# Kernel tuning notes

Measured on AMD Instinct MI355X. Metric: run time of the kernel, lower is better.

## Reference

```python
import jax, jax.numpy as jnp
import numpy as np

D = 1024
H = 16
HD = D // H


def setup_inputs() -> dict:
    key = jax.random.key(0)
    ks = jax.random.split(key, 9)
    s = 1.0 / np.sqrt(D)
    x = jax.random.normal(ks[0], (2, 2048, D), dtype=jnp.float32)
    Wq = jax.random.uniform(ks[1], (D, D), jnp.float32, -s, s)
    bq = jax.random.uniform(ks[2], (D,), jnp.float32, -s, s)
    Wk = jax.random.uniform(ks[3], (D, D), jnp.float32, -s, s)
    bk = jax.random.uniform(ks[4], (D,), jnp.float32, -s, s)
    Wv = jax.random.uniform(ks[5], (D, D), jnp.float32, -s, s)
    bv = jax.random.uniform(ks[6], (D,), jnp.float32, -s, s)
    Wo = jax.random.uniform(ks[7], (D, D), jnp.float32, -s, s)
    bo = jax.random.uniform(ks[8], (D,), jnp.float32, -s, s)
    return {"x": x, "Wq": Wq, "bq": bq, "Wk": Wk, "bk": bk,
            "Wv": Wv, "bv": bv, "Wo": Wo, "bo": bo}


def reference(x, Wq, bq, Wk, bk, Wv, bv, Wo, bo):
    B, S, _ = x.shape
    # project and split heads -> [B, H, S, HD]
    def split(t):
        return t.reshape(B, S, H, HD).transpose(0, 2, 1, 3)
    q = split(x @ Wq + bq)
    k = split(x @ Wk + bk)
    v = split(x @ Wv + bv)
    scores = jnp.einsum('bhqd,bhkd->bhqk', q, k) / np.sqrt(HD).astype(np.float32)
    attn = jax.nn.softmax(scores, axis=-1)
    ctx = jnp.einsum('bhqk,bhkd->bhqd', attn, v)  # [B,H,S,HD]
    ctx = ctx.transpose(0, 2, 1, 3).reshape(B, S, D)
    return ctx @ Wo + bo
```

## Files before the change

### kernel.cpp

```cpp
#include <hip/hip_runtime.h>
#include <hip/hip_bf16.h>
#include <math.h>

#define BB 2
#define SS 2048
#define DD 1024
#define HH 16
#define HD 64
#define MM (BB * SS)
#define NT (SS / 64)

typedef __bf16 bf16;
typedef __attribute__((ext_vector_type(8))) __bf16 bf16x8;
typedef __attribute__((ext_vector_type(4))) __bf16 bf16x4;
typedef __attribute__((ext_vector_type(4))) float f32x4;
typedef __attribute__((ext_vector_type(4))) unsigned u32x4;

#define QSCL 0.18033688011112042f

__device__ __forceinline__ void glds16(const bf16* g, bf16* l) {
    __builtin_amdgcn_global_load_lds(
        (const __attribute__((address_space(1))) void*)g,
        (__attribute__((address_space(3))) void*)l, 16, 0, 0);
}

__device__ __forceinline__ unsigned cvtpk_bf16(float a, float b) {
    unsigned r;
    asm("v_cvt_pk_bf16_f32 %0, %1, %2" : "=v"(r) : "v"(a), "v"(b));
    return r;
}

__global__ __launch_bounds__(256) void cvt_x(const float* __restrict__ x,
                                             bf16* __restrict__ xb) {
    int i = (blockIdx.x * 256 + threadIdx.x) * 4;
    float4 v = *(const float4*)(x + i);
    bf16x4 o;
    o[0] = (bf16)v.x; o[1] = (bf16)v.y; o[2] = (bf16)v.z; o[3] = (bf16)v.w;
    *(bf16x4*)(xb + i) = o;
}

__global__ __launch_bounds__(256) void cvt_w(
    const float* __restrict__ W0, const float* __restrict__ W1,
    const float* __restrict__ W2, const float* __restrict__ W3,
    bf16* __restrict__ Wt) {
    const float* W = (blockIdx.z == 0) ? W0 : (blockIdx.z == 1) ? W1
                   : (blockIdx.z == 2) ? W2 : W3;
    bf16* dst = Wt + (size_t)blockIdx.z * DD * DD;

    __shared__ float T[64][65];
    int k0 = blockIdx.y * 64, n0 = blockIdx.x * 64;
    int tr = threadIdx.x >> 4, tc = (threadIdx.x & 15) * 4;
#pragma unroll
    for (int u = 0; u < 4; u++) {
        int r = tr + u * 16;
        float4 v = *(const float4*)&W[(size_t)(k0 + r) * DD + n0 + tc];
        T[tc + 0][r] = v.x; T[tc + 1][r] = v.y;
        T[tc + 2][r] = v.z; T[tc + 3][r] = v.w;
    }
    __syncthreads();
#pragma unroll
    for (int u = 0; u < 4; u++) {
        int r = tr + u * 16;
        bf16x4 o;
        o[0] = (bf16)T[r][tc + 0]; o[1] = (bf16)T[r][tc + 1];
        o[2] = (bf16)T[r][tc + 2]; o[3] = (bf16)T[r][tc + 3];
        *(bf16x4*)&dst[(size_t)(n0 + r) * DD + k0 + tc] = o;
    }
}

__global__ __launch_bounds__(256) void vt_kernel(const bf16* __restrict__ V,
                                                 bf16* __restrict__ Vt) {
    const int bh = blockIdx.y;
    const int b = bh >> 4, h = bh & 15;
    const int s0 = blockIdx.x * 64;

    __shared__ bf16 T[64][72];
    const int r = threadIdx.x >> 2;
    const int C = threadIdx.x & 3;
    const int c0 = C * 16;

    const bf16* src = V + ((size_t)(b * SS + s0 + r)) * DD + h * HD + c0;
    *(bf16x8*)&T[r][c0]     = *(const bf16x8*)(src);
    *(bf16x8*)&T[r][c0 + 8] = *(const bf16x8*)(src + 8);
    __syncthreads();

    const int M0 = (C >> 1) * 32 + (C & 1) * 8;
    bf16x8 o0, o1;
#pragma unroll
    for (int i = 0; i < 4; i++) o0[i]     = T[M0 + i][r];
#pragma unroll
    for (int i = 0; i < 4; i++) o0[4 + i] = T[M0 + 16 + i][r];
#pragma unroll
    for (int i = 0; i < 4; i++) o1[i]     = T[M0 + 4 + i][r];
#pragma unroll
    for (int i = 0; i < 4; i++) o1[4 + i] = T[M0 + 20 + i][r];
    bf16* dst = Vt + ((size_t)bh * HD + r) * SS + s0 + c0;
    *(bf16x8*)dst       = o0;
    *(bf16x8*)(dst + 8) = o1;
}

__global__ __launch_bounds__(256) void mfma_gemm(
    const bf16* __restrict__ A, const bf16* __restrict__ Wt0,
    const float* __restrict__ b0, const float* __restrict__ b1,
    const float* __restrict__ b2,
    bf16* __restrict__ o0, bf16* __restrict__ o1, bf16* __restrict__ o2) {
    const int z = blockIdx.z;
    const bf16* Wt = Wt0 + (size_t)z * DD * DD;
    const float* bias = (z == 0) ? b0 : (z == 1) ? b1 : b2;
    bf16* dstb = (z == 0) ? o0 : (z == 1) ? o1 : o2;
    const float scl = (z == 0) ? QSCL : 1.0f;

    __shared__ __align__(16) bf16 As[128 * 64];
    __shared__ __align__(16) bf16 Bs[128 * 64];

    const int tid = threadIdx.x;
    const int lane = tid & 63;
    const int w = tid >> 6;
    const int l15 = lane & 15, quad = lane >> 4;
    const int m0 = blockIdx.y * 128;
    const int n0 = blockIdx.x * 128;
    const int mw = (w & 1) * 64;
    const int nw = (w >> 1) * 64;

    f32x4 acc[4][4];
#pragma unroll
    for (int i = 0; i < 4; i++)
#pragma unroll
        for (int j = 0; j < 4; j++) acc[i][j] = (f32x4){0.f, 0.f, 0.f, 0.f};

    for (int kt = 0; kt < DD; kt += 64) {
        __syncthreads();
#pragma unroll
        for (int u = 0; u < 4; u++) {
            int j = tid + u * 256;
            int row = j >> 3, cp = j & 7;
            int c = cp ^ (row & 7);
            glds16(A  + (size_t)(m0 + row) * DD + kt + c * 8, &As[j * 8]);
            glds16(Wt + (size_t)(n0 + row) * DD + kt + c * 8, &Bs[j * 8]);
        }
        __syncthreads();

#pragma unroll
        for (int kh = 0; kh < 2; kh++) {
            bf16x8 af[4], bf[4];
#pragma unroll
            for (int i = 0; i < 4; i++) {
                int ra = mw + i * 16 + l15;
                int ja = ra * 8 + ((kh * 4 + quad) ^ (ra & 7));
                af[i] = *(const bf16x8*)&As[ja * 8];
                int rb = nw + i * 16 + l15;
                int jb = rb * 8 + ((kh * 4 + quad) ^ (rb & 7));
                bf[i] = *(const bf16x8*)&Bs[jb * 8];
            }
#pragma unroll
            for (int i = 0; i < 4; i++)
#pragma unroll
                for (int j = 0; j < 4; j++)
                    acc[i][j] = __builtin_amdgcn_mfma_f32_16x16x32_bf16(
                        af[i], bf[j], acc[i][j], 0, 0, 0);
        }
    }

    float bcol[4];
#pragma unroll
    for (int j = 0; j < 4; j++) bcol[j] = bias[n0 + nw + j * 16 + l15];

#pragma unroll
    for (int i = 0; i < 4; i++)
#pragma unroll
        for (int j = 0; j < 4; j++)
#pragma unroll
            for (int r = 0; r < 4; r++) {
                int row = m0 + mw + i * 16 + quad * 4 + r;
                int col = n0 + nw + j * 16 + l15;
                dstb[(size_t)row * DD + col] =
                    (bf16)((acc[i][j][r] + bcol[j]) * scl);
            }
}

__global__ __launch_bounds__(256) void mfma_gemm_out(
    const bf16* __restrict__ A, const bf16* __restrict__ Wt,
    const float* __restrict__ bias, float* __restrict__ out) {
    __shared__ __align__(16) bf16 As[64 * 64];
    __shared__ __align__(16) bf16 Bs[128 * 64];

    const int tid = threadIdx.x;
    const int lane = tid & 63;
    const int w = tid >> 6;
    const int l15 = lane & 15, quad = lane >> 4;
    const int m0 = blockIdx.y * 64;
    const int n0 = blockIdx.x * 128;
    const int mw = (w & 1) * 32;
    const int nw = (w >> 1) * 64;

    f32x4 acc[2][4];
#pragma unroll
    for (int i = 0; i < 2; i++)
#pragma unroll
        for (int j = 0; j < 4; j++) acc[i][j] = (f32x4){0.f, 0.f, 0.f, 0.f};

    for (int kt = 0; kt < DD; kt += 64) {
        __syncthreads();
#pragma unroll
        for (int u = 0; u < 2; u++) {
            int j = tid + u * 256;
            int row = j >> 3, c = (j & 7) ^ (row & 7);
            glds16(A + (size_t)(m0 + row) * DD + kt + c * 8, &As[j * 8]);
        }
#pragma unroll
        for (int u = 0; u < 4; u++) {
            int j = tid + u * 256;
            int row = j >> 3, c = (j & 7) ^ (row & 7);
            glds16(Wt + (size_t)(n0 + row) * DD + kt + c * 8, &Bs[j * 8]);
        }
        __syncthreads();

#pragma unroll
        for (int kh = 0; kh < 2; kh++) {
            bf16x8 af[2], bf[4];
#pragma unroll
            for (int i = 0; i < 2; i++) {
                int ra = mw + i * 16 + l15;
                int ja = ra * 8 + ((kh * 4 + quad) ^ (ra & 7));
                af[i] = *(const bf16x8*)&As[ja * 8];
            }
#pragma unroll
            for (int j = 0; j < 4; j++) {
                int rb = nw + j * 16 + l15;
                int jb = rb * 8 + ((kh * 4 + quad) ^ (rb & 7));
                bf[j] = *(const bf16x8*)&Bs[jb * 8];
            }
#pragma unroll
            for (int i = 0; i < 2; i++)
#pragma unroll
                for (int j = 0; j < 4; j++)
                    acc[i][j] = __builtin_amdgcn_mfma_f32_16x16x32_bf16(
                        af[i], bf[j], acc[i][j], 0, 0, 0);
        }
    }

    float bcol[4];
#pragma unroll
    for (int j = 0; j < 4; j++) bcol[j] = bias[n0 + nw + j * 16 + l15];

#pragma unroll
    for (int i = 0; i < 2; i++)
#pragma unroll
        for (int j = 0; j < 4; j++)
#pragma unroll
            for (int r = 0; r < 4; r++) {
                int row = m0 + mw + i * 16 + quad * 4 + r;
                int col = n0 + nw + j * 16 + l15;
                out[(size_t)row * DD + col] = acc[i][j][r] + bcol[j];
            }
}

__global__ __launch_bounds__(256) void mfma_attn(
    const bf16* __restrict__ Qb, const bf16* __restrict__ Kb,
    const bf16* __restrict__ Vtg, bf16* __restrict__ ctxb) {
    __shared__ __align__(16) bf16 Ks[2][64 * 64];
    __shared__ __align__(16) bf16 Vs[2][64 * 64];

    const int tid = threadIdx.x;
    const int lane = tid & 63;
    const int w = tid >> 6;
    const int l15 = lane & 15, quad = lane >> 4;
    const int bh = blockIdx.y;
    const int b = bh >> 4, h = bh & 15;
    const int q0 = blockIdx.x * 64;
    const size_t mb = (size_t)b * SS;
    const int hc = h * HD;
    const bf16* Vt_bh = Vtg + (size_t)bh * HD * SS;

    bf16x8 qf[2];
#pragma unroll
    for (int kh = 0; kh < 2; kh++)
        qf[kh] = *(const bf16x8*)&Qb[(mb + q0 + w * 16 + l15) * DD +
                                     hc + kh * 32 + quad * 8];

    bf16x8 onev;
#pragma unroll
    for (int i = 0; i < 8; i++) onev[i] = (bf16)1.0f;

    int koff[4][2], voff[4][2];
#pragma unroll
    for (int kb = 0; kb < 4; kb++) {
        int rk = kb * 16 + l15;
#pragma unroll
        for (int kh = 0; kh < 2; kh++)
            koff[kb][kh] = (rk * 8 + ((kh * 4 + quad) ^ (rk & 7))) * 8;
    }
#pragma unroll
    for (int nb = 0; nb < 4; nb++) {
        int rv = nb * 16 + l15;
#pragma unroll
        for (int kh = 0; kh < 2; kh++)
            voff[nb][kh] = (rv * 8 + ((kh * 4 + quad) ^ (rv & 7))) * 8;
    }

    const bf16* gK[2]; const bf16* gV[2]; int lo_[2];
#pragma unroll
    for (int u = 0; u < 2; u++) {
        int j = tid + u * 256;
        int row = j >> 3, cp = j & 7;
        int c = cp ^ (row & 7);
        gK[u] = Kb + (mb + row) * DD + hc + c * 8;
        gV[u] = Vt_bh + (size_t)row * SS + c * 8;
        lo_[u] = j * 8;
    }

    f32x4 o[4], lsum;
    lsum = (f32x4){0.f, 0.f, 0.f, 0.f};
#pragma unroll
    for (int nb = 0; nb < 4; nb++) o[nb] = (f32x4){0.f, 0.f, 0.f, 0.f};

#pragma unroll
    for (int u = 0; u < 2; u++) {
        glds16(gK[u], &Ks[0][lo_[u]]);  gK[u] += 64 * DD;
        glds16(gV[u], &Vs[0][lo_[u]]);  gV[u] += 64;
    }
    __syncthreads();

    f32x4 scA[4];
#pragma unroll
    for (int kb = 0; kb < 4; kb++) scA[kb] = (f32x4){0.f, 0.f, 0.f, 0.f};
#pragma unroll
    for (int kb = 0; kb < 4; kb++)
#pragma unroll
        for (int kh = 0; kh < 2; kh++) {
            bf16x8 kf = *(const bf16x8*)&Ks[0][koff[kb][kh]];
            scA[kb] = __builtin_amdgcn_mfma_f32_16x16x32_bf16(
                kf, qf[kh], scA[kb], 0, 0, 0);
        }

    int buf = 0;
    for (int it = 0; it < NT; ++it) {
        const bool more = (it + 1 < NT);
        if (more) {
#pragma unroll
            for (int u = 0; u < 2; u++) {
                glds16(gK[u], &Ks[buf ^ 1][lo_[u]]);  gK[u] += 64 * DD;
                glds16(gV[u], &Vs[buf ^ 1][lo_[u]]);  gV[u] += 64;
            }
        }

        u32x4 pw[2];
#pragma unroll
        for (int kb = 0; kb < 4; kb++) {
            float p0 = exp2f(scA[kb][0]);
            float p1 = exp2f(scA[kb][1]);
            float p2 = exp2f(scA[kb][2]);
            float p3 = exp2f(scA[kb][3]);
            pw[kb >> 1][(kb & 1) * 2 + 0] = cvtpk_bf16(p0, p1);
            pw[kb >> 1][(kb & 1) * 2 + 1] = cvtpk_bf16(p2, p3);
        }
        bf16x8 pfr[2];
        pfr[0] = __builtin_bit_cast(bf16x8, pw[0]);
        pfr[1] = __builtin_bit_cast(bf16x8, pw[1]);

        __syncthreads();

        __builtin_amdgcn_s_setprio(1);
        f32x4 scB[4];
#pragma unroll
        for (int kb = 0; kb < 4; kb++) scB[kb] = (f32x4){0.f, 0.f, 0.f, 0.f};
        if (more) {
#pragma unroll
            for (int kb = 0; kb < 4; kb++)
#pragma unroll
                for (int kh = 0; kh < 2; kh++) {
                    bf16x8 kf = *(const bf16x8*)&Ks[buf ^ 1][koff[kb][kh]];
                    scB[kb] = __builtin_amdgcn_mfma_f32_16x16x32_bf16(
                        kf, qf[kh], scB[kb], 0, 0, 0);
                }
        }
#pragma unroll
        for (int kh = 0; kh < 2; kh++) {
            lsum = __builtin_amdgcn_mfma_f32_16x16x32_bf16(
                pfr[kh], onev, lsum, 0, 0, 0);
#pragma unroll
            for (int nb = 0; nb < 4; nb++) {
                bf16x8 vf = *(const bf16x8*)&Vs[buf][voff[nb][kh]];
                o[nb] = __builtin_amdgcn_mfma_f32_16x16x32_bf16(
                    pfr[kh], vf, o[nb], 0, 0, 0);
            }
        }
        __builtin_amdgcn_s_setprio(0);

        __syncthreads();

#pragma unroll
        for (int kb = 0; kb < 4; kb++) scA[kb] = scB[kb];
        buf ^= 1;
    }

    float li[4];
#pragma unroll
    for (int r = 0; r < 4; r++) li[r] = 1.0f / lsum[r];
#pragma unroll
    for (int nb = 0; nb < 4; nb++)
#pragma unroll
        for (int r = 0; r < 4; r++) {
            int qrow = q0 + w * 16 + quad * 4 + r;
            ctxb[(mb + qrow) * DD + hc + nb * 16 + l15] =
                (bf16)(o[nb][r] * li[r]);
        }
}

extern "C" void kernel_launch(void* const* d_in, const int* in_sizes, int n_in,
                              void* d_out, int out_size, void* d_ws, size_t ws_size,
                              hipStream_t stream) {
    const float* x  = (const float*)d_in[0];
    const float* Wq = (const float*)d_in[1];
    const float* bq = (const float*)d_in[2];
    const float* Wk = (const float*)d_in[3];
    const float* bk = (const float*)d_in[4];
    const float* Wv = (const float*)d_in[5];
    const float* bv = (const float*)d_in[6];
    const float* Wo = (const float*)d_in[7];
    const float* bo = (const float*)d_in[8];
    float* out = (float*)d_out;

    char* base = (char*)d_ws;
    bf16* xb   = (bf16*)(base);
    bf16* Wt   = (bf16*)(base + (8ull  << 20));
    bf16* Qb   = (bf16*)(base + (16ull << 20));
    bf16* Kb   = (bf16*)(base + (24ull << 20));
    bf16* Vb   = (bf16*)(base + (32ull << 20));
    bf16* ctxb = (bf16*)(base + (40ull << 20));
    bf16* Vtg  = xb;

    cvt_x<<<dim3((MM * DD) / (256 * 4)), dim3(256), 0, stream>>>(x, xb);
    cvt_w<<<dim3(16, 16, 4), dim3(256), 0, stream>>>(Wq, Wk, Wv, Wo, Wt);

    mfma_gemm<<<dim3(DD / 128, MM / 128, 3), dim3(256), 0, stream>>>(
        xb, Wt, bq, bk, bv, Qb, Kb, Vb);

    vt_kernel<<<dim3(SS / 64, BB * HH), dim3(256), 0, stream>>>(Vb, Vtg);

    mfma_attn<<<dim3(SS / 64, BB * HH), dim3(256), 0, stream>>>(Qb, Kb, Vtg, ctxb);

    mfma_gemm_out<<<dim3(DD / 128, MM / 64), dim3(256), 0, stream>>>(
        ctxb, Wt + 3ull * DD * DD, bo, out);
}
```

Before: 220.5 us.

## Fuse V transpose into QKV GEMM epilogue and merge conversion kernels

The V projection GEMM now writes its output directly in the permuted per-head transposed layout the attention kernel consumes, which removes the separate vt_kernel pass and its extra read and write of V. The x and weight conversion kernels are merged into a single launch, saving one launch. The attention score MFMAs now start from a zero constant instead of zero-initialised accumulators, and the score copy is skipped on the last iteration. The transposed epilogue writes 4-element strided chunks, which may coalesce less well than the original row-major stores.

New measurement: 219.4 us. No clear change (-0.5%).

```diff
diff --git a/kernel.cpp b/kernel.cpp
--- a/kernel.cpp
+++ b/kernel.cpp
@@ -30,25 +30,26 @@
     return r;
 }
 
-__global__ __launch_bounds__(256) void cvt_x(const float* __restrict__ x,
-                                             bf16* __restrict__ xb) {
-    int i = (blockIdx.x * 256 + threadIdx.x) * 4;
-    float4 v = *(const float4*)(x + i);
-    bf16x4 o;
-    o[0] = (bf16)v.x; o[1] = (bf16)v.y; o[2] = (bf16)v.z; o[3] = (bf16)v.w;
-    *(bf16x4*)(xb + i) = o;
-}
-
-__global__ __launch_bounds__(256) void cvt_w(
+__global__ __launch_bounds__(256) void cvt_prep(
+    const float* __restrict__ x, bf16* __restrict__ xb,
     const float* __restrict__ W0, const float* __restrict__ W1,
     const float* __restrict__ W2, const float* __restrict__ W3,
     bf16* __restrict__ Wt) {
-    const float* W = (blockIdx.z == 0) ? W0 : (blockIdx.z == 1) ? W1
-                   : (blockIdx.z == 2) ? W2 : W3;
-    bf16* dst = Wt + (size_t)blockIdx.z * DD * DD;
-
     __shared__ float T[64][65];
-    int k0 = blockIdx.y * 64, n0 = blockIdx.x * 64;
+    const int bid = blockIdx.x;
+    if (bid < 4096) {
+        int i = (bid * 256 + threadIdx.x) * 4;
+        float4 v = *(const float4*)(x + i);
+        bf16x4 o;
+        o[0] = (bf16)v.x; o[1] = (bf16)v.y; o[2] = (bf16)v.z; o[3] = (bf16)v.w;
+        *(bf16x4*)(xb + i) = o;
+        return;
+    }
+    const int b = bid - 4096;
+    const int z = b >> 8;
+    const float* W = (z == 0) ? W0 : (z == 1) ? W1 : (z == 2) ? W2 : W3;
+    bf16* dst = Wt + (size_t)z * DD * DD;
+    int k0 = ((b >> 4) & 15) * 64, n0 = (b & 15) * 64;
     int tr = threadIdx.x >> 4, tc = (threadIdx.x & 15) * 4;
 #pragma unroll
     for (int u = 0; u < 4; u++) {
@@ -66,37 +67,6 @@
         o[2] = (bf16)T[r][tc + 2]; o[3] = (bf16)T[r][tc + 3];
         *(bf16x4*)&dst[(size_t)(n0 + r) * DD + k0 + tc] = o;
     }
-}
-
-__global__ __launch_bounds__(256) void vt_kernel(const bf16* __restrict__ V,
-                                                 bf16* __restrict__ Vt) {
-    const int bh = blockIdx.y;
-    const int b = bh >> 4, h = bh & 15;
-    const int s0 = blockIdx.x * 64;
-
-    __shared__ bf16 T[64][72];
-    const int r = threadIdx.x >> 2;
-    const int C = threadIdx.x & 3;
-    const int c0 = C * 16;
-
-    const bf16* src = V + ((size_t)(b * SS + s0 + r)) * DD + h * HD + c0;
-    *(bf16x8*)&T[r][c0]     = *(const bf16x8*)(src);
-    *(bf16x8*)&T[r][c0 + 8] = *(const bf16x8*)(src + 8);
-    __syncthreads();
-
-    const int M0 = (C >> 1) * 32 + (C & 1) * 8;
-    bf16x8 o0, o1;
-#pragma unroll
-    for (int i = 0; i < 4; i++) o0[i]     = T[M0 + i][r];
-#pragma unroll
-    for (int i = 0; i < 4; i++) o0[4 + i] = T[M0 + 16 + i][r];
-#pragma unroll
-    for (int i = 0; i < 4; i++) o1[i]     = T[M0 + 4 + i][r];
-#pragma unroll
-    for (int i = 0; i < 4; i++) o1[4 + i] = T[M0 + 20 + i][r];
-    bf16* dst = Vt + ((size_t)bh * HD + r) * SS + s0 + c0;
-    *(bf16x8*)dst       = o0;
-    *(bf16x8*)(dst + 8) = o1;
 }
 
 __global__ __launch_bounds__(256) void mfma_gemm(
@@ -107,7 +77,6 @@
     const int z = blockIdx.z;
     const bf16* Wt = Wt0 + (size_t)z * DD * DD;
     const float* bias = (z == 0) ? b0 : (z == 1) ? b1 : b2;
-    bf16* dstb = (z == 0) ? o0 : (z == 1) ? o1 : o2;
     const float scl = (z == 0) ? QSCL : 1.0f;
 
     __shared__ __align__(16) bf16 As[128 * 64];
@@ -165,17 +134,39 @@
 #pragma unroll
     for (int j = 0; j < 4; j++) bcol[j] = bias[n0 + nw + j * 16 + l15];
 
-#pragma unroll
-    for (int i = 0; i < 4; i++)
-#pragma unroll
-        for (int j = 0; j < 4; j++)
-#pragma unroll
-            for (int r = 0; r < 4; r++) {
-                int row = m0 + mw + i * 16 + quad * 4 + r;
-                int col = n0 + nw + j * 16 + l15;
-                dstb[(size_t)row * DD + col] =
-                    (bf16)((acc[i][j][r] + bcol[j]) * scl);
-            }
+    if (z == 2) {
+        const int mbase = m0 + mw;
+        const int bb = (mbase >= SS) ? 1 : 0;
+        const int sw = mbase & (SS - 1);
+#pragma unroll
+        for (int i = 0; i < 4; i++) {
+            int scol = sw + (i >> 1) * 32 + quad * 8 + (i & 1) * 4;
+#pragma unroll
+            for (int j = 0; j < 4; j++) {
+                int dg = n0 + nw + j * 16 + l15;
+                int h = dg >> 6, d = dg & 63;
+                bf16* dst = o2 + ((size_t)(bb * HH + h) * HD + d) * SS + scol;
+                bf16x4 ov;
+#pragma unroll
+                for (int r = 0; r < 4; r++)
+                    ov[r] = (bf16)(acc[i][j][r] + bcol[j]);
+                *(bf16x4*)dst = ov;
+            }
+        }
+    } else {
+        bf16* dstb = (z == 0) ? o0 : o1;
+#pragma unroll
+        for (int i = 0; i < 4; i++)
+#pragma unroll
+            for (int j = 0; j < 4; j++)
+#pragma unroll
+                for (int r = 0; r < 4; r++) {
+                    int row = m0 + mw + i * 16 + quad * 4 + r;
+                    int col = n0 + nw + j * 16 + l15;
+                    dstb[(size_t)row * DD + col] =
+                        (bf16)((acc[i][j][r] + bcol[j]) * scl);
+                }
+    }
 }
 
 __global__ __launch_bounds__(256) void mfma_gemm_out(
@@ -281,6 +272,7 @@
     bf16x8 onev;
 #pragma unroll
     for (int i = 0; i < 8; i++) onev[i] = (bf16)1.0f;
+    const f32x4 zf = (f32x4){0.f, 0.f, 0.f, 0.f};
 
     int koff[4][2], voff[4][2];
 #pragma unroll
@@ -323,15 +315,14 @@
 
     f32x4 scA[4];
 #pragma unroll
-    for (int kb = 0; kb < 4; kb++) scA[kb] = (f32x4){0.f, 0.f, 0.f, 0.f};
-#pragma unroll
-    for (int kb = 0; kb < 4; kb++)
-#pragma unroll
-        for (int kh = 0; kh < 2; kh++) {
-            bf16x8 kf = *(const bf16x8*)&Ks[0][koff[kb][kh]];
-            scA[kb] = __builtin_amdgcn_mfma_f32_16x16x32_bf16(
-                kf, qf[kh], scA[kb], 0, 0, 0);
-        }
+    for (int kb = 0; kb < 4; kb++) {
+        bf16x8 kf0 = *(const bf16x8*)&Ks[0][koff[kb][0]];
+        bf16x8 kf1 = *(const bf16x8*)&Ks[0][koff[kb][1]];
+        f32x4 t = __builtin_amdgcn_mfma_f32_16x16x32_bf16(
+            kf0, qf[0], zf, 0, 0, 0);
+        scA[kb] = __builtin_amdgcn_mfma_f32_16x16x32_bf16(
+            kf1, qf[1], t, 0, 0, 0);
+    }
 
     int buf = 0;
     for (int it = 0; it < NT; ++it) {
@@ -362,17 +353,16 @@
 
         __builtin_amdgcn_s_setprio(1);
         f32x4 scB[4];
-#pragma unroll
-        for (int kb = 0; kb < 4; kb++) scB[kb] = (f32x4){0.f, 0.f, 0.f, 0.f};
         if (more) {
 #pragma unroll
-            for (int kb = 0; kb < 4; kb++)
-#pragma unroll
-                for (int kh = 0; kh < 2; kh++) {
-                    bf16x8 kf = *(const bf16x8*)&Ks[buf ^ 1][koff[kb][kh]];
-                    scB[kb] = __builtin_amdgcn_mfma_f32_16x16x32_bf16(
-                        kf, qf[kh], scB[kb], 0, 0, 0);
-                }
+            for (int kb = 0; kb < 4; kb++) {
+                bf16x8 kf0 = *(const bf16x8*)&Ks[buf ^ 1][koff[kb][0]];
+                bf16x8 kf1 = *(const bf16x8*)&Ks[buf ^ 1][koff[kb][1]];
+                f32x4 t = __builtin_amdgcn_mfma_f32_16x16x32_bf16(
+                    kf0, qf[0], zf, 0, 0, 0);
+                scB[kb] = __builtin_amdgcn_mfma_f32_16x16x32_bf16(
+                    kf1, qf[1], t, 0, 0, 0);
+            }
         }
 #pragma unroll
         for (int kh = 0; kh < 2; kh++) {
@@ -389,8 +379,10 @@
 
         __syncthreads();
 
-#pragma unroll
-        for (int kb = 0; kb < 4; kb++) scA[kb] = scB[kb];
+        if (more) {
+#pragma unroll
+            for (int kb = 0; kb < 4; kb++) scA[kb] = scB[kb];
+        }
         buf ^= 1;
     }
 
@@ -426,19 +418,16 @@
     bf16* Wt   = (bf16*)(base + (8ull  << 20));
     bf16* Qb   = (bf16*)(base + (16ull << 20));
     bf16* Kb   = (bf16*)(base + (24ull << 20));
-    bf16* Vb   = (bf16*)(base + (32ull << 20));
+    bf16* Vt   = (bf16*)(base + (32ull << 20));
     bf16* ctxb = (bf16*)(base + (40ull << 20));
-    bf16* Vtg  = xb;
-
-    cvt_x<<<dim3((MM * DD) / (256 * 4)), dim3(256), 0, stream>>>(x, xb);
-    cvt_w<<<dim3(16, 16, 4), dim3(256), 0, stream>>>(Wq, Wk, Wv, Wo, Wt);
+
+    cvt_prep<<<dim3(4096 + 1024), dim3(256), 0, stream>>>(
+        x, xb, Wq, Wk, Wv, Wo, Wt);
 
     mfma_gemm<<<dim3(DD / 128, MM / 128, 3), dim3(256), 0, stream>>>(
-        xb, Wt, bq, bk, bv, Qb, Kb, Vb);
-
-    vt_kernel<<<dim3(SS / 64, BB * HH), dim3(256), 0, stream>>>(Vb, Vtg);
-
-    mfma_attn<<<dim3(SS / 64, BB * HH), dim3(256), 0, stream>>>(Qb, Kb, Vtg, ctxb);
+        xb, Wt, bq, bk, bv, Qb, Kb, Vt);
+
+    mfma_attn<<<dim3(SS / 64, BB * HH), dim3(256), 0, stream>>>(Qb, Kb, Vt, ctxb);
 
     mfma_gemm_out<<<dim3(DD / 128, MM / 64), dim3(256), 0, stream>>>(
         ctxb, Wt + 3ull * DD * DD, bo, out);
```
